# Kernel tuning notes

Measured on AMD Instinct MI355X. Metric: run time of the kernel, lower is better.

The kernel has to match this reference:

```python
import jax, jax.numpy as jnp
import numpy as np
import math

# config constants (match init_kwargs)
N_HEAD = 16
KNN_NUM = 4
MEM_FRAC = 4.0
BOOKKEEPING_FRAC = 0.0
RESID_ONLY = False
RESID_FOUND = 0.5   # set_resid_frac(resid_frac): found/current mix
RESID_CURR = 0.5
KNN_INFLUENCE = 1.0
NEG_INF = jnp.finfo(jnp.float32).min


def setup_inputs() -> dict:
    key = jax.random.key(0)
    k1, k2, k3, k4, k5 = jax.random.split(key, 5)
    B, T, C = 1, 2048, 1024
    H, d = N_HEAD, C // N_HEAD
    M = 8192  # per-head memory-store entries
    return {
        "x": jax.random.normal(k1, (B, T, C), jnp.float32),
        "c_attn_w": jax.random.normal(k2, (3 * C, C), jnp.float32) * 0.02,
        "c_proj_w": jax.random.normal(k3, (C, C), jnp.float32) * 0.02,
        "key_store": jax.random.normal(k4, (H, M, d), jnp.float32),
        "value_store": jax.random.normal(k5, (H, M, d), jnp.float32),
    }


def _knn_get(att, k, q, v, key_store, value_store):
    # att: (B,H,T,T), k/q/v: (B,H,T,d), stores: (H,M,d). B must be 1 (original
    # scatter offset i*t is only consistent for b==1).
    B, H, T, d = k.shape
    scale = 1.0 / math.sqrt(d)
    att_last = att[:, :, -1, :]                     # (B,H,T) last-query column
    # bookkeeping_frac == 0.0 -> skipped; mem_frac truthy -> threshold filter
    mask = att_last >= (1.0 / (MEM_FRAC * T))       # nonzero after zeroing

    # per-head flattened token lists, shape (H, N=B*T, d)
    kh = jnp.swapaxes(k, 0, 1).reshape(H, B * T, d)
    qh = jnp.swapaxes(q, 0, 1).reshape(H, B * T, d)
    vh = jnp.swapaxes(v, 0, 1).reshape(H, B * T, d)
    mask_h = jnp.swapaxes(mask, 0, 1).reshape(H, B * T)

    # exact L2 kNN (FAISS IndexFlatL2 equivalent): d2[h,n,m] = ||kh - ks||^2
    d2 = (jnp.sum(kh * kh, -1)[:, :, None]
          - 2.0 * jnp.einsum('hnd,hmd->hnm', kh, key_store)
          + jnp.sum(key_store * key_store, -1)[:, None, :])
    _, idx = jax.lax.top_k(-d2, KNN_NUM)            # (H,N,K) nearest indices

    h_ix = jnp.arange(H)[:, None, None]
    keys_found = key_store[h_ix, idx]               # (H,N,K,d)
    vals_found = value_store[h_ix, idx]
    keys_found = jnp.moveaxis(keys_found, 2, 0)     # (K,H,N,d)
    vals_found = jnp.moveaxis(vals_found, 2, 0)
    if not RESID_ONLY:
        keys_found = jnp.concatenate([kh[None], keys_found], axis=0)  # (K+1,H,N,d)
        vals_found = jnp.concatenate([vh[None], vals_found], axis=0)

    attf = jnp.einsum('khnd,hnd->khn', keys_found, qh) * scale
    attf = jnp.where(jnp.isnan(attf), NEG_INF, attf)
    attf = jax.nn.softmax(attf * KNN_INFLUENCE, axis=0)
    vals_new = jnp.einsum('khn,khnd->hnd', attf, vals_found)
    if RESID_FOUND > 0 or RESID_CURR > 0:
        vals_new = vals_new * RESID_FOUND + vh * RESID_CURR

    v_out = jnp.where(mask_h[..., None], vals_new, vh)   # scatter-equivalent
    return jnp.swapaxes(v_out.reshape(H, B, T, d), 0, 1)  # (B,H,T,d)


def reference(x, c_attn_w, c_proj_w, key_store, value_store):
    B, T, C = x.shape
    H, d = N_HEAD, C // N_HEAD
    qkv = x @ c_attn_w.T                             # (B,T,3C)
    q, k, v = jnp.split(qkv, 3, axis=2)
    q = jnp.swapaxes(q.reshape(B, T, H, d), 1, 2)    # (B,H,T,d)
    k = jnp.swapaxes(k.reshape(B, T, H, d), 1, 2)
    v = jnp.swapaxes(v.reshape(B, T, H, d), 1, 2)

    att = jnp.einsum('bhqd,bhkd->bhqk', q, k) * (1.0 / math.sqrt(d))
    causal = jnp.tril(jnp.ones((T, T), bool))
    att = jnp.where(causal, att, NEG_INF)
    att = jax.nn.softmax(att, axis=-1)

    # knn_get is @torch.no_grad() in the original -> stop_gradient
    v_new = jax.lax.stop_gradient(
        _knn_get(att, k, q, v, key_store, value_store))

    y = jnp.einsum('bhqk,bhkd->bhqd', att, v_new)
    y = jnp.swapaxes(y, 1, 2).reshape(B, T, C)
    return y @ c_proj_w.T
```

## Files before the change

### kernel.cpp

```cpp
#include <hip/hip_runtime.h>
#include <hip/hip_bf16.h>
#include <math.h>

#define TT 2048
#define CC 1024
#define HH 16
#define DDIM 64
#define MM 8192
#define C3 3072
#define SBIAS 256.0f

#define LTPAIR(sa,ma,sb,mb) ((sa) < (sb) || ((sa) == (sb) && (ma) < (mb)))

typedef __bf16 bf16x8 __attribute__((ext_vector_type(8)));
typedef float f32x4 __attribute__((ext_vector_type(4)));

__device__ __forceinline__ float waveReduceSum(float v) {
#pragma unroll
  for (int off = 32; off > 0; off >>= 1) v += __shfl_xor(v, off, 64);
  return v;
}
__device__ __forceinline__ unsigned waveMinU32(unsigned v) {
#pragma unroll
  for (int off = 32; off > 0; off >>= 1) {
    unsigned o = __shfl_xor(v, off, 64);
    v = (o < v) ? o : v;
  }
  return v;
}
__device__ __forceinline__ unsigned umn(unsigned a, unsigned b){ return a<b?a:b; }
__device__ __forceinline__ unsigned umx(unsigned a, unsigned b){ return a>b?a:b; }

__device__ __forceinline__ void gload16(const void* g, void* l) {
  __builtin_amdgcn_global_load_lds(
      (const __attribute__((address_space(1))) unsigned int*)g,
      (__attribute__((address_space(3))) unsigned int*)l, 16, 0, 0);
}

__global__ __launch_bounds__(256) void conv_split_k(const float* __restrict__ src,
    __hip_bfloat16* __restrict__ hi, __hip_bfloat16* __restrict__ lo)
{
  size_t i = (size_t)blockIdx.x*256 + threadIdx.x;
  const float4* p = (const float4*)(src + i*8);
  float4 a = p[0], b = p[1];
  float v[8] = {a.x,a.y,a.z,a.w,b.x,b.y,b.z,b.w};
  bf16x8 H, L;
#pragma unroll
  for (int e = 0; e < 8; ++e) {
    __bf16 hb = (__bf16)v[e];
    H[e] = hb;
    L[e] = (__bf16)(v[e] - (float)hb);
  }
  *reinterpret_cast<bf16x8*>(hi + i*8) = H;
  *reinterpret_cast<bf16x8*>(lo + i*8) = L;
}

__global__ __launch_bounds__(256) void conv_bf16_k(const float* __restrict__ src,
    __hip_bfloat16* __restrict__ dst)
{
  size_t i = (size_t)blockIdx.x*256 + threadIdx.x;
  const float4* p = (const float4*)(src + i*8);
  float4 a = p[0], b = p[1];
  float v[8] = {a.x,a.y,a.z,a.w,b.x,b.y,b.z,b.w};
  bf16x8 H;
#pragma unroll
  for (int e = 0; e < 8; ++e) H[e] = (__bf16)v[e];
  *reinterpret_cast<bf16x8*>(dst + i*8) = H;
}

__global__ __launch_bounds__(256) void conv_ks_k(const float* __restrict__ ks,
    __hip_bfloat16* __restrict__ ksb, float* __restrict__ ksn, float* __restrict__ ksnb)
{
  int row = blockIdx.x*4 + (threadIdx.x>>6);
  int lane = threadIdx.x & 63;
  float v = ks[(size_t)row*64 + lane];
  float sq = waveReduceSum(v*v);
  ksb[(size_t)row*64 + lane] = __float2bfloat16(v);
  if (lane == 0) { ksn[row] = sq; ksnb[row] = sq + SBIAS; }
}

__global__ __launch_bounds__(256) void conv_kb_k(const float* __restrict__ qkv,
    __hip_bfloat16* __restrict__ kb)
{
  int e = blockIdx.x*256 + threadIdx.x;
  int dg = e & 7; int t = (e>>3) & (TT-1); int h = e >> 14;
  const float* src = qkv + (size_t)t*C3 + CC + h*64 + dg*8;
  __hip_bfloat16* dst = kb + ((size_t)(h*TT + t)*64 + dg*8);
#pragma unroll
  for (int i = 0; i < 8; ++i) dst[i] = __float2bfloat16(src[i]);
}

__global__ __launch_bounds__(256) void vtrans_k(const float* __restrict__ vnew,
    __hip_bfloat16* __restrict__ vbT)
{
  __shared__ float tbuf[64][65];
  const int h = blockIdx.y, t0 = blockIdx.x*64, tid = threadIdx.x;
#pragma unroll
  for (int r = 0; r < 16; ++r) {
    int e = r*256 + tid; int row = e>>6, dv = e&63;
    tbuf[row][dv] = vnew[((size_t)h*TT + t0 + row)*64 + dv];
  }
  __syncthreads();
#pragma unroll
  for (int r = 0; r < 16; ++r) {
    int e = r*256 + tid; int dv = e>>6, tt = e&63;
    vbT[((size_t)h*64 + dv)*TT + t0 + tt] = __float2bfloat16(tbuf[tt][dv]);
  }
}

template<bool SPLIT>
__global__ __launch_bounds__(256) void gemm_mfma_k(
    const __hip_bfloat16* __restrict__ Ah, const __hip_bfloat16* __restrict__ Al,
    const __hip_bfloat16* __restrict__ Bh, const __hip_bfloat16* __restrict__ Bl,
    float* __restrict__ Cc, int M, int N, int K)
{
  __shared__ __align__(16) char lds[2][32768];
  const int tid = threadIdx.x;
  const int nbx = N >> 7;
  const int by = blockIdx.x / nbx, bx = blockIdx.x - by*nbx;
  const int m0 = by << 7, n0 = bx << 7;
  const int w = tid >> 6;
  const int l = tid & 63;
  const int wslot = w << 6;
  const int wi = w >> 1, wj = w & 1;
  const int fr = l & 15, fo = l >> 4;
  const int kw = SPLIT ? 32 : 64;
  const int nsteps = K / kw;

  f32x4 acc[4][4];
#pragma unroll
  for (int i = 0; i < 4; ++i)
#pragma unroll
    for (int j = 0; j < 4; ++j) acc[i][j] = f32x4{0.f,0.f,0.f,0.f};

  int srow[4], schg[4];
#pragma unroll
  for (int r = 0; r < 4; ++r) {
    int s = r*256 + tid;
    srow[r] = s >> 3;
    schg[r] = (s & 7) ^ (srow[r] & 7);
  }

  auto stageAB = [&](int buf, int st) {
    const int k0 = st * kw;
#pragma unroll
    for (int r = 0; r < 4; ++r) {
      const __hip_bfloat16 *pa, *pb;
      if (SPLIT) {
        pa = (schg[r] < 4 ? Ah : Al) + (size_t)(m0+srow[r])*K + k0 + (schg[r]&3)*8;
        pb = (schg[r] < 4 ? Bh : Bl) + (size_t)(n0+srow[r])*K + k0 + (schg[r]&3)*8;
      } else {
        pa = Ah + (size_t)(m0+srow[r])*K + k0 + schg[r]*8;
        pb = Bh + (size_t)(n0+srow[r])*K + k0 + schg[r]*8;
      }
      gload16(pa, lds[buf] + (r*256 + wslot)*16);
      gload16(pb, lds[buf] + 16384 + (r*256 + wslot)*16);
    }
  };

  stageAB(0, 0);
  __syncthreads();

  for (int st = 0; st < nsteps; ++st) {
    const int buf = st & 1;
    if (st + 1 < nsteps) stageAB(buf ^ 1, st + 1);
    char* ldsb = lds[buf];

    if (SPLIT) {
      bf16x8 bhf[4], blf[4];
#pragma unroll
      for (int j = 0; j < 4; ++j) {
        int row = wj*64 + j*16 + fr;
        bhf[j] = *(const bf16x8*)(ldsb + 16384 + row*128 + ((fo     ^ (row&7))*16));
        blf[j] = *(const bf16x8*)(ldsb + 16384 + row*128 + (((4+fo) ^ (row&7))*16));
      }
#pragma unroll
      for (int i = 0; i < 4; ++i) {
        int row = wi*64 + i*16 + fr;
        bf16x8 ah = *(const bf16x8*)(ldsb + row*128 + ((fo     ^ (row&7))*16));
        bf16x8 al = *(const bf16x8*)(ldsb + row*128 + (((4+fo) ^ (row&7))*16));
#pragma unroll
        for (int j = 0; j < 4; ++j) {
          acc[i][j] = __builtin_amdgcn_mfma_f32_16x16x32_bf16(al, bhf[j], acc[i][j], 0,0,0);
          acc[i][j] = __builtin_amdgcn_mfma_f32_16x16x32_bf16(ah, blf[j], acc[i][j], 0,0,0);
          acc[i][j] = __builtin_amdgcn_mfma_f32_16x16x32_bf16(ah, bhf[j], acc[i][j], 0,0,0);
        }
      }
    } else {
#pragma unroll
      for (int kk = 0; kk < 2; ++kk) {
        bf16x8 bf[4];
#pragma unroll
        for (int j = 0; j < 4; ++j) {
          int row = wj*64 + j*16 + fr;
          bf[j] = *(const bf16x8*)(ldsb + 16384 + row*128 + (((kk*4+fo) ^ (row&7))*16));
        }
#pragma unroll
        for (int i = 0; i < 4; ++i) {
          int row = wi*64 + i*16 + fr;
          bf16x8 af = *(const bf16x8*)(ldsb + row*128 + (((kk*4+fo) ^ (row&7))*16));
#pragma unroll
          for (int j = 0; j < 4; ++j)
            acc[i][j] = __builtin_amdgcn_mfma_f32_16x16x32_bf16(af, bf[j], acc[i][j], 0,0,0);
        }
      }
    }
    __syncthreads();
  }

  float* ep = (float*)((char*)lds + (size_t)w*8704);
#pragma unroll
  for (int pass = 0; pass < 2; ++pass) {
#pragma unroll
    for (int ii = 0; ii < 2; ++ii) {
      int i = pass*2 + ii;
#pragma unroll
      for (int j = 0; j < 4; ++j)
#pragma unroll
        for (int e = 0; e < 4; ++e)
          ep[(ii*16 + fo*4 + e)*68 + j*16 + fr] = acc[i][j][e];
    }
#pragma unroll
    for (int eidx = 0; eidx < 8; ++eidx) {
      int fi = eidx*64 + l;
      int row = fi >> 4, c4 = fi & 15;
      float4 v4 = *(const float4*)(ep + row*68 + c4*4);
      *(float4*)(Cc + (size_t)(m0 + wi*64 + pass*32 + row)*N + n0 + wj*64 + c4*4) = v4;
    }
  }
}

__global__ __launch_bounds__(256) void attlast_mask_k(const float* __restrict__ qkv, int* __restrict__ mask)
{
  const int h = blockIdx.x;
  __shared__ float ql[64];
  __shared__ float lg[TT];
  __shared__ float red[256];
  const int tid = threadIdx.x;
  if (tid < 64) ql[tid] = qkv[(size_t)(TT-1)*C3 + h*DDIM + tid];
  __syncthreads();
  float lmax = -INFINITY;
  for (int t = tid; t < TT; t += 256) {
    const float* kr = qkv + (size_t)t*C3 + CC + h*DDIM;
    float s = 0.f;
#pragma unroll
    for (int d = 0; d < 64; ++d) s += ql[d] * kr[d];
    s *= 0.125f;
    lg[t] = s;
    lmax = fmaxf(lmax, s);
  }
  red[tid] = lmax; __syncthreads();
  for (int off = 128; off > 0; off >>= 1) { if (tid < off) red[tid] = fmaxf(red[tid], red[tid+off]); __syncthreads(); }
  float mx = red[0];
  __syncthreads();
  float ls = 0.f;
  for (int t = tid; t < TT; t += 256) { float e = expf(lg[t]-mx); lg[t] = e; ls += e; }
  red[tid] = ls; __syncthreads();
  for (int off = 128; off > 0; off >>= 1) { if (tid < off) red[tid] += red[tid+off]; __syncthreads(); }
  float Z = red[0];
  for (int t = tid; t < TT; t += 256) mask[h*TT + t] = (lg[t]/Z >= 1.220703125e-4f) ? 1 : 0;
}

__global__ __launch_bounds__(256) void knn_chunkmin_k(
    const __hip_bfloat16* __restrict__ kb, const __hip_bfloat16* __restrict__ ksb,
    const float* __restrict__ ksnb, unsigned int* __restrict__ cand)
{
  __shared__ __align__(16) char lds[2*8192];
  const int tid = threadIdx.x;
  const int bid = blockIdx.x;
  const int orig = (bid & 7)*64 + (bid >> 3);
  const int h  = orig >> 5;
  const int n0 = (orig & 31) * 64;
  const int w  = tid >> 6;
  const int l  = tid & 63;
  const int cr = l & 15, hi = l >> 4;

  bf16x8 af0, af1;
  {
    const __hip_bfloat16* kbh = kb + (size_t)h*TT*64 + (size_t)(n0 + w*16 + cr)*64;
    af0 = *reinterpret_cast<const bf16x8*>(kbh + 0*32 + hi*8);
    af1 = *reinterpret_cast<const bf16x8*>(kbh + 1*32 + hi*8);
  }
  const __hip_bfloat16* ksbh = ksb + (size_t)h*MM*64;
  const float* ksnh = ksnb + (size_t)h*MM;

  const int c0 = tid*2, c1 = tid*2 + 1;
  const int wb0 = (c0>>3)*128 + (((c0&7) ^ ((c0>>3)&7))*16);
  const int wb1 = (c1>>3)*128 + (((c1&7) ^ ((c1>>3)&7))*16);
  const int rb0 = (l&15)*128 + (((0 + hi) ^ (l&7))*16);
  const int rb1 = (l&15)*128 + (((4 + hi) ^ (l&7))*16);

  unsigned cnd[4][4];
#pragma unroll
  for (int i = 0; i < 4; ++i)
#pragma unroll
    for (int c = 0; c < 4; ++c) cnd[i][c] = 0xFFFFFFFFu;

  uint4 r0, r1;
  {
    const uint4* g = reinterpret_cast<const uint4*>(ksbh);
    r0 = g[c0]; r1 = g[c1];
    *reinterpret_cast<uint4*>(lds + wb0) = r0;
    *reinterpret_cast<uint4*>(lds + wb1) = r1;
  }

  for (int tt = 0; tt < 128; ++tt) {
    __syncthreads();
    const int buf = tt & 1;
    char* ldsb = lds + buf*8192;
    if (tt + 1 < 128) {
      const uint4* g = reinterpret_cast<const uint4*>(ksbh + (size_t)(tt+1)*64*64);
      r0 = g[c0]; r1 = g[c1];
    }
    float kn0 = ksnh[tt*64 +  0 + cr];
    float kn1 = ksnh[tt*64 + 16 + cr];
    float kn2 = ksnh[tt*64 + 32 + cr];
    float kn3 = ksnh[tt*64 + 48 + cr];

    f32x4 acc[4];
#pragma unroll
    for (int b = 0; b < 4; ++b) {
      bf16x8 bf0 = *reinterpret_cast<const bf16x8*>(ldsb + b*2048 + rb0);
      bf16x8 bf1 = *reinterpret_cast<const bf16x8*>(ldsb + b*2048 + rb1);
      f32x4 z = {0.f, 0.f, 0.f, 0.f};
      z = __builtin_amdgcn_mfma_f32_16x16x32_bf16(af0, bf0, z, 0, 0, 0);
      z = __builtin_amdgcn_mfma_f32_16x16x32_bf16(af1, bf1, z, 0, 0, 0);
      acc[b] = z;
    }
#pragma unroll
    for (int i = 0; i < 4; ++i) {
      float s0 = fmaf(acc[0][i], -2.f, kn0);
      float s1 = fmaf(acc[1][i], -2.f, kn1);
      float s2 = fmaf(acc[2][i], -2.f, kn2);
      float s3 = fmaf(acc[3][i], -2.f, kn3);
      float m4 = fminf(fminf(s0, s1), fminf(s2, s3));
      unsigned x = (__float_as_uint(m4) & 0xFFFFFF80u) | (unsigned)tt;
      unsigned tmp;
      tmp = umn(cnd[i][0], x); x = umx(cnd[i][0], x); cnd[i][0] = tmp;
      tmp = umn(cnd[i][1], x); x = umx(cnd[i][1], x); cnd[i][1] = tmp;
      tmp = umn(cnd[i][2], x); x = umx(cnd[i][2], x); cnd[i][2] = tmp;
      cnd[i][3] = umn(cnd[i][3], x);
    }
    if (tt + 1 < 128) {
      char* ldsn = lds + (buf^1)*8192;
      *reinterpret_cast<uint4*>(ldsn + wb0) = r0;
      *reinterpret_cast<uint4*>(ldsn + wb1) = r1;
    }
  }

#pragma unroll
  for (int i = 0; i < 4; ++i) {
    int n = n0 + w*16 + hi*4 + i;
    reinterpret_cast<uint4*>(cand)[(size_t)(h*TT + n)*16 + cr] =
        make_uint4(cnd[i][0], cnd[i][1], cnd[i][2], cnd[i][3]);
  }
}

__global__ __launch_bounds__(256) void knn_select_k(
    const unsigned int* __restrict__ cand, const float* __restrict__ qkv,
    const float* __restrict__ kstore, const float* __restrict__ ksn,
    int* __restrict__ idxout)
{
  const int row = blockIdx.x*4 + (threadIdx.x>>6);
  const int l = threadIdx.x & 63;
  const int h = row >> 11, t = row & (TT-1);
  unsigned v = cand[(size_t)row*64 + (l&15)*4 + (l>>4)];
  const float kreg = qkv[(size_t)t*C3 + CC + h*64 + l];
  const float* ksh = kstore + (size_t)h*MM*64;
  const float* ksnh = ksn + (size_t)h*MM;

  float bs0=3.4e38f, bs1=3.4e38f, bs2=3.4e38f, bs3=3.4e38f;
  int bm0=0x7fffffff, bm1=0x7fffffff, bm2=0x7fffffff, bm3=0x7fffffff;

  for (int it = 0; it < 8; ++it) {
    unsigned mv = waveMinU32(v);
    if (mv == 0xFFFFFFFFu) break;
    unsigned long long ball = __ballot(v == mv);
    int src = __ffsll(ball) - 1;
    int tIdx = (int)(mv & 127u);
    int crw = src & 15;
    if (l == src) v = 0xFFFFFFFFu;
#pragma unroll
    for (int b = 0; b < 4; ++b) {
      int m = tIdx*64 + b*16 + crw;
      float ksv = ksh[(size_t)m*64 + l];
      float dot = waveReduceSum(kreg * ksv);
      float s = ksnh[m] - 2.f*dot;
      if (LTPAIR(s,m, bs3,bm3)) {
        if (LTPAIR(s,m, bs1,bm1)) {
          bs3=bs2; bm3=bm2; bs2=bs1; bm2=bm1;
          if (LTPAIR(s,m, bs0,bm0)) { bs1=bs0; bm1=bm0; bs0=s; bm0=m; }
          else { bs1=s; bm1=m; }
        } else {
          if (LTPAIR(s,m, bs2,bm2)) { bs3=bs2; bm3=bm2; bs2=s; bm2=m; }
          else { bs3=s; bm3=m; }
        }
      }
    }
  }
  if (l == 0) {
    int* o = idxout + (size_t)row*4;
    o[0]=bm0; o[1]=bm1; o[2]=bm2; o[3]=bm3;
  }
}

__global__ __launch_bounds__(256) void knn_apply_k(
    const float* __restrict__ qkv, const float* __restrict__ kstore, const float* __restrict__ vstore,
    const int* __restrict__ idx, const int* __restrict__ mask, float* __restrict__ vnew)
{
  const int r = blockIdx.x * 4 + (threadIdx.x >> 6);
  const int lane = threadIdx.x & 63;
  const int h = r >> 11, t = r & (TT-1);
  const float* base = qkv + (size_t)t*C3 + h*DDIM;
  float vh = base[2*CC + lane];
  float* outp = vnew + ((size_t)h*TT + t)*DDIM;
  if (!mask[r]) { outp[lane] = vh; return; }
  float qd = base[lane];
  float kd = base[CC + lane];
  float s0 = waveReduceSum(qd*kd) * 0.125f;
  float sj[4], vj[4];
#pragma unroll
  for (int j = 0; j < 4; ++j) {
    int m = idx[(size_t)r*4 + j];
    const float* kp = kstore + ((size_t)h*MM + m)*DDIM;
    const float* vp = vstore + ((size_t)h*MM + m)*DDIM;
    sj[j] = waveReduceSum(qd * kp[lane]) * 0.125f;
    vj[j] = vp[lane];
  }
  float mx = fmaxf(fmaxf(fmaxf(s0,sj[0]),fmaxf(sj[1],sj[2])),sj[3]);
  float w0 = expf(s0-mx), w1 = expf(sj[0]-mx), w2 = expf(sj[1]-mx), w3 = expf(sj[2]-mx), w4 = expf(sj[3]-mx);
  float Z = w0+w1+w2+w3+w4;
  float vnw = (w0*vh + w1*vj[0] + w2*vj[1] + w3*vj[2] + w4*vj[3]) / Z;
  outp[lane] = 0.5f*vnw + 0.5f*vh;
}

__global__ __launch_bounds__(256) void attn_mfma_k(
    const float* __restrict__ qkv, const __hip_bfloat16* __restrict__ kb,
    const __hip_bfloat16* __restrict__ vbT, __hip_bfloat16* __restrict__ yb)
{
  __shared__ __align__(16) char lds[40960];
  const int h = blockIdx.y, bx = blockIdx.x, tid = threadIdx.x;
  const int w = tid>>6, l = tid&63, fr = l&15, fo = l>>4;
  const int wslot = w << 6;
  const __hip_bfloat16* kbh = kb + (size_t)h*TT*64;
  const __hip_bfloat16* vbh = vbT + (size_t)h*64*TT;
  char* Pt = lds + 32768 + w*2048;

  int srow[2], schg[2];
#pragma unroll
  for (int r = 0; r < 2; ++r) {
    int s = r*256 + tid;
    srow[r] = s >> 3;
    schg[r] = (s & 7) ^ (srow[r] & 7);
  }

  auto stageKV = [&](int buf, int kt) {
#pragma unroll
    for (int r = 0; r < 2; ++r) {
      gload16(kbh + (size_t)(kt*64 + srow[r])*64 + schg[r]*8,
              lds + buf*16384 + (r*256 + wslot)*16);
      gload16(vbh + (size_t)srow[r]*TT + kt*64 + schg[r]*8,
              lds + buf*16384 + 8192 + (r*256 + wslot)*16);
    }
  };

  for (int half = 0; half < 2; ++half) {
    const int qblk = half ? (31 - bx) : bx;
    const int q0 = qblk * 64;
    bf16x8 qa[2];
    {
      const float* qrow = qkv + (size_t)(q0 + w*16 + fr)*C3 + h*64;
#pragma unroll
      for (int kk = 0; kk < 2; ++kk) {
        float4 u0 = *(const float4*)(qrow + kk*32 + fo*8);
        float4 u1 = *(const float4*)(qrow + kk*32 + fo*8 + 4);
        bf16x8 t;
        t[0]=(__bf16)u0.x; t[1]=(__bf16)u0.y; t[2]=(__bf16)u0.z; t[3]=(__bf16)u0.w;
        t[4]=(__bf16)u1.x; t[5]=(__bf16)u1.y; t[6]=(__bf16)u1.z; t[7]=(__bf16)u1.w;
        qa[kk] = t;
      }
    }
    float mrow[4], lsum[4];
    f32x4 oacc[4];
#pragma unroll
    for (int e = 0; e < 4; ++e) { mrow[e] = -INFINITY; lsum[e] = 0.f; }
#pragma unroll
    for (int jv = 0; jv < 4; ++jv) oacc[jv] = f32x4{0.f,0.f,0.f,0.f};

    const int ntiles = qblk + 1;
    stageKV(0, 0);
    __syncthreads();

    for (int kt = 0; kt < ntiles; ++kt) {
      const int buf = kt & 1;
      if (kt + 1 < ntiles) stageKV(buf ^ 1, kt + 1);
      char* Kt = lds + buf*16384;
      char* Vt = Kt + 8192;

      f32x4 sv[4];
#pragma unroll
      for (int j = 0; j < 4; ++j) {
        int row = j*16 + fr;
        bf16x8 k0f = *(const bf16x8*)(Kt + row*128 + ((fo     ^ (row&7))*16));
        bf16x8 k1f = *(const bf16x8*)(Kt + row*128 + (((4+fo) ^ (row&7))*16));
        f32x4 z = {0.f,0.f,0.f,0.f};
        z = __builtin_amdgcn_mfma_f32_16x16x32_bf16(qa[0], k0f, z, 0,0,0);
        z = __builtin_amdgcn_mfma_f32_16x16x32_bf16(qa[1], k1f, z, 0,0,0);
        sv[j] = z;
      }
      if (kt == qblk) {
#pragma unroll
        for (int j = 0; j < 4; ++j)
#pragma unroll
          for (int e = 0; e < 4; ++e)
            sv[j][e] = (j*16 + fr <= w*16 + fo*4 + e) ? sv[j][e]*0.125f : -INFINITY;
      } else {
#pragma unroll
        for (int j = 0; j < 4; ++j)
#pragma unroll
          for (int e = 0; e < 4; ++e) sv[j][e] *= 0.125f;
      }
      float rmax[4];
#pragma unroll
      for (int e = 0; e < 4; ++e)
        rmax[e] = fmaxf(fmaxf(sv[0][e], sv[1][e]), fmaxf(sv[2][e], sv[3][e]));
#pragma unroll
      for (int off = 1; off < 16; off <<= 1)
#pragma unroll
        for (int e = 0; e < 4; ++e) rmax[e] = fmaxf(rmax[e], __shfl_xor(rmax[e], off, 64));
      float scl[4];
#pragma unroll
      for (int e = 0; e < 4; ++e) {
        float mn = fmaxf(mrow[e], rmax[e]);
        scl[e] = __expf(mrow[e] - mn);
        mrow[e] = mn;
      }
      float rsum[4] = {0.f,0.f,0.f,0.f};
#pragma unroll
      for (int j = 0; j < 4; ++j) {
        int chunkbase = j*2 + (fr>>3);
        int kvoff = (fr&7)*2;
#pragma unroll
        for (int e = 0; e < 4; ++e) {
          float p = __expf(sv[j][e] - mrow[e]);
          rsum[e] += p;
          int qloc = fo*4 + e;
          *(__bf16*)(Pt + qloc*128 + ((chunkbase ^ (qloc&7))*16) + kvoff) = (__bf16)p;
        }
      }
#pragma unroll
      for (int off = 1; off < 16; off <<= 1)
#pragma unroll
        for (int e = 0; e < 4; ++e) rsum[e] += __shfl_xor(rsum[e], off, 64);
#pragma unroll
      for (int e = 0; e < 4; ++e) lsum[e] = lsum[e]*scl[e] + rsum[e];
#pragma unroll
      for (int jv = 0; jv < 4; ++jv)
#pragma unroll
        for (int e = 0; e < 4; ++e) oacc[jv][e] *= scl[e];

      bf16x8 pa0 = *(const bf16x8*)(Pt + fr*128 + ((fo     ^ (fr&7))*16));
      bf16x8 pa1 = *(const bf16x8*)(Pt + fr*128 + (((4+fo) ^ (fr&7))*16));
#pragma unroll
      for (int jv = 0; jv < 4; ++jv) {
        int row = jv*16 + fr;
        bf16x8 v0f = *(const bf16x8*)(Vt + row*128 + ((fo     ^ (row&7))*16));
        bf16x8 v1f = *(const bf16x8*)(Vt + row*128 + (((4+fo) ^ (row&7))*16));
        oacc[jv] = __builtin_amdgcn_mfma_f32_16x16x32_bf16(pa0, v0f, oacc[jv], 0,0,0);
        oacc[jv] = __builtin_amdgcn_mfma_f32_16x16x32_bf16(pa1, v1f, oacc[jv], 0,0,0);
      }
      __syncthreads();
    }
#pragma unroll
    for (int jv = 0; jv < 4; ++jv)
#pragma unroll
      for (int e = 0; e < 4; ++e) {
        int t = q0 + w*16 + fo*4 + e;
        yb[(size_t)t*CC + h*64 + jv*16 + fr] = __float2bfloat16(oacc[jv][e] / lsum[e]);
      }
  }
}

extern "C" void kernel_launch(void* const* d_in, const int* in_sizes, int n_in,
                              void* d_out, int out_size, void* d_ws, size_t ws_size,
                              hipStream_t stream) {
  const float* x   = (const float*)d_in[0];
  const float* wat = (const float*)d_in[1];
  const float* wpr = (const float*)d_in[2];
  const float* kst = (const float*)d_in[3];
  const float* vst = (const float*)d_in[4];
  float* out = (float*)d_out;

  float* ws    = (float*)d_ws;
  float* qkv   = ws;
  float* ksn   = qkv + (size_t)6291456;
  float* ksnb  = ksn + 131072;
  int*   idxb  = (int*)(ksnb + 131072);
  int*   maskb = idxb + 131072;
  __hip_bfloat16* kb = (__hip_bfloat16*)(maskb + 32768);
  float* candRegion = (float*)kb + 1048576;
  unsigned int* candb = (unsigned int*)candRegion;
  float* vnew = candRegion;
  __hip_bfloat16* vbT = (__hip_bfloat16*)(candRegion + 2097152);
  float* split = candRegion + 2097152 + 1048576;
  __hip_bfloat16* xhi = (__hip_bfloat16*)split;
  __hip_bfloat16* xlo = xhi + 2097152;
  __hip_bfloat16* whi = xlo + 2097152;
  __hip_bfloat16* wlo = whi + 3145728;
  __hip_bfloat16* ksb  = (__hip_bfloat16*)split;
  __hip_bfloat16* wprb = ksb + 8388608;
  __hip_bfloat16* yb   = (__hip_bfloat16*)split;

  conv_split_k<<<dim3(1024), 256, 0, stream>>>(x, xhi, xlo);
  conv_split_k<<<dim3(1536), 256, 0, stream>>>(wat, whi, wlo);
  gemm_mfma_k<true><<<dim3(16*24), 256, 0, stream>>>(xhi, xlo, whi, wlo, qkv, TT, C3, CC);
  conv_kb_k<<<dim3(1024), 256, 0, stream>>>(qkv, kb);
  conv_ks_k<<<dim3(HH*MM/4), 256, 0, stream>>>(kst, ksb, ksn, ksnb);
  conv_bf16_k<<<dim3(512), 256, 0, stream>>>(wpr, wprb);
  attlast_mask_k<<<dim3(HH), 256, 0, stream>>>(qkv, maskb);
  knn_chunkmin_k<<<dim3(512), 256, 0, stream>>>(kb, ksb, ksnb, candb);
  knn_select_k<<<dim3(HH*TT/4), 256, 0, stream>>>(candb, qkv, kst, ksn, idxb);
  knn_apply_k<<<dim3(HH*TT/4), 256, 0, stream>>>(qkv, kst, vst, idxb, maskb, vnew);
  vtrans_k<<<dim3(32, HH), 256, 0, stream>>>(vnew, vbT);
  attn_mfma_k<<<dim3(16, HH), 256, 0, stream>>>(qkv, kb, vbT, yb);
  gemm_mfma_k<false><<<dim3(16*8), 256, 0, stream>>>(yb, nullptr, wprb, nullptr, out, TT, CC, CC);
}
```

Measured before the change: 352.4 us.

## Fuse kNN select and apply kernels with wave-wide bitonic candidate sort

Merges the kNN candidate-selection and value-apply kernels into one kernel and skips the selection work for rows whose mask is zero. The serial 8-iteration wave-min loop, with its per-candidate wave reductions, is replaced by a bitonic sort across the wave. Each lane pair then computes one exact fp32 distance, and a second bitonic sort on (score, index) keys picks the top four. The candidate encoding now packs the column-within-chunk bits into the key, which lowers the float precision kept in the first-pass ranking. That could change which candidates reach exact rescoring. It also drops the intermediate index buffer and one kernel launch.

```diff
diff --git a/kernel.cpp b/kernel.cpp
--- a/kernel.cpp
+++ b/kernel.cpp
@@ -10,22 +10,12 @@
 #define C3 3072
 #define SBIAS 256.0f
 
-#define LTPAIR(sa,ma,sb,mb) ((sa) < (sb) || ((sa) == (sb) && (ma) < (mb)))
-
 typedef __bf16 bf16x8 __attribute__((ext_vector_type(8)));
 typedef float f32x4 __attribute__((ext_vector_type(4)));
 
 __device__ __forceinline__ float waveReduceSum(float v) {
 #pragma unroll
   for (int off = 32; off > 0; off >>= 1) v += __shfl_xor(v, off, 64);
-  return v;
-}
-__device__ __forceinline__ unsigned waveMinU32(unsigned v) {
-#pragma unroll
-  for (int off = 32; off > 0; off >>= 1) {
-    unsigned o = __shfl_xor(v, off, 64);
-    v = (o < v) ? o : v;
-  }
   return v;
 }
 __device__ __forceinline__ unsigned umn(unsigned a, unsigned b){ return a<b?a:b; }
@@ -274,6 +264,7 @@
   const int w  = tid >> 6;
   const int l  = tid & 63;
   const int cr = l & 15, hi = l >> 4;
+  const unsigned crbits = (unsigned)cr << 7;
 
   bf16x8 af0, af1;
   {
@@ -334,7 +325,7 @@
       float s2 = fmaf(acc[2][i], -2.f, kn2);
       float s3 = fmaf(acc[3][i], -2.f, kn3);
       float m4 = fminf(fminf(s0, s1), fminf(s2, s3));
-      unsigned x = (__float_as_uint(m4) & 0xFFFFFF80u) | (unsigned)tt;
+      unsigned x = (__float_as_uint(m4) & 0xFFFFF800u) | crbits | (unsigned)tt;
       unsigned tmp;
       tmp = umn(cnd[i][0], x); x = umx(cnd[i][0], x); cnd[i][0] = tmp;
       tmp = umn(cnd[i][1], x); x = umx(cnd[i][1], x); cnd[i][1] = tmp;
@@ -356,82 +347,100 @@
   }
 }
 
-__global__ __launch_bounds__(256) void knn_select_k(
+__global__ __launch_bounds__(256) void knn_fused_k(
     const unsigned int* __restrict__ cand, const float* __restrict__ qkv,
-    const float* __restrict__ kstore, const float* __restrict__ ksn,
-    int* __restrict__ idxout)
+    const float* __restrict__ kstore, const float* __restrict__ vstore,
+    const float* __restrict__ ksn, const int* __restrict__ mask,
+    float* __restrict__ vnew)
 {
   const int row = blockIdx.x*4 + (threadIdx.x>>6);
   const int l = threadIdx.x & 63;
   const int h = row >> 11, t = row & (TT-1);
-  unsigned v = cand[(size_t)row*64 + (l&15)*4 + (l>>4)];
-  const float kreg = qkv[(size_t)t*C3 + CC + h*64 + l];
-  const float* ksh = kstore + (size_t)h*MM*64;
-  const float* ksnh = ksn + (size_t)h*MM;
-
-  float bs0=3.4e38f, bs1=3.4e38f, bs2=3.4e38f, bs3=3.4e38f;
-  int bm0=0x7fffffff, bm1=0x7fffffff, bm2=0x7fffffff, bm3=0x7fffffff;
-
-  for (int it = 0; it < 8; ++it) {
-    unsigned mv = waveMinU32(v);
-    if (mv == 0xFFFFFFFFu) break;
-    unsigned long long ball = __ballot(v == mv);
-    int src = __ffsll(ball) - 1;
-    int tIdx = (int)(mv & 127u);
-    int crw = src & 15;
-    if (l == src) v = 0xFFFFFFFFu;
-#pragma unroll
-    for (int b = 0; b < 4; ++b) {
-      int m = tIdx*64 + b*16 + crw;
-      float ksv = ksh[(size_t)m*64 + l];
-      float dot = waveReduceSum(kreg * ksv);
-      float s = ksnh[m] - 2.f*dot;
-      if (LTPAIR(s,m, bs3,bm3)) {
-        if (LTPAIR(s,m, bs1,bm1)) {
-          bs3=bs2; bm3=bm2; bs2=bs1; bm2=bm1;
-          if (LTPAIR(s,m, bs0,bm0)) { bs1=bs0; bm1=bm0; bs0=s; bm0=m; }
-          else { bs1=s; bm1=m; }
-        } else {
-          if (LTPAIR(s,m, bs2,bm2)) { bs3=bs2; bm3=bm2; bs2=s; bm2=m; }
-          else { bs3=s; bm3=m; }
-        }
-      }
-    }
-  }
-  if (l == 0) {
-    int* o = idxout + (size_t)row*4;
-    o[0]=bm0; o[1]=bm1; o[2]=bm2; o[3]=bm3;
-  }
-}
-
-__global__ __launch_bounds__(256) void knn_apply_k(
-    const float* __restrict__ qkv, const float* __restrict__ kstore, const float* __restrict__ vstore,
-    const int* __restrict__ idx, const int* __restrict__ mask, float* __restrict__ vnew)
-{
-  const int r = blockIdx.x * 4 + (threadIdx.x >> 6);
-  const int lane = threadIdx.x & 63;
-  const int h = r >> 11, t = r & (TT-1);
-  const float* base = qkv + (size_t)t*C3 + h*DDIM;
-  float vh = base[2*CC + lane];
-  float* outp = vnew + ((size_t)h*TT + t)*DDIM;
-  if (!mask[r]) { outp[lane] = vh; return; }
-  float qd = base[lane];
-  float kd = base[CC + lane];
-  float s0 = waveReduceSum(qd*kd) * 0.125f;
-  float sj[4], vj[4];
-#pragma unroll
-  for (int j = 0; j < 4; ++j) {
-    int m = idx[(size_t)r*4 + j];
-    const float* kp = kstore + ((size_t)h*MM + m)*DDIM;
-    const float* vp = vstore + ((size_t)h*MM + m)*DDIM;
-    sj[j] = waveReduceSum(qd * kp[lane]) * 0.125f;
-    vj[j] = vp[lane];
-  }
-  float mx = fmaxf(fmaxf(fmaxf(s0,sj[0]),fmaxf(sj[1],sj[2])),sj[3]);
-  float w0 = expf(s0-mx), w1 = expf(sj[0]-mx), w2 = expf(sj[1]-mx), w3 = expf(sj[2]-mx), w4 = expf(sj[3]-mx);
+  const float* base = qkv + (size_t)t*C3 + h*64;
+  float vh = base[2*CC + l];
+  float* outp = vnew + (size_t)row*64;
+  if (!mask[row]) { outp[l] = vh; return; }
+
+  unsigned v = cand[(size_t)row*64 + l];
+#pragma unroll
+  for (int k = 2; k <= 64; k <<= 1)
+#pragma unroll
+    for (int j = k>>1; j > 0; j >>= 1) {
+      unsigned o = __shfl_xor(v, j, 64);
+      bool takeMin = ((l & j) == 0) == ((l & k) == 0);
+      v = (takeMin == (o < v)) ? o : v;
+    }
+
+  const int c = l >> 1;
+  const int b = c & 3;
+  unsigned vc = __shfl(v, c >> 2, 64);
+  const int m = ((int)(vc & 127u))*64 + b*16 + (int)((vc >> 7) & 15u);
+  const int p = l & 1;
+  {
+    const float* kq = base + CC + p*32;
+    const float* ksr = kstore + ((size_t)h*MM + m)*64 + p*32;
+    float dp = 0.f;
+#pragma unroll
+    for (int i = 0; i < 8; ++i) {
+      float4 a = *(const float4*)(kq + i*4);
+      float4 bb = *(const float4*)(ksr + i*4);
+      dp = fmaf(a.x,bb.x, fmaf(a.y,bb.y, fmaf(a.z,bb.z, fmaf(a.w,bb.w, dp))));
+    }
+    dp += __shfl_xor(dp, 1, 64);
+    float s = ksn[(size_t)h*MM + m] - 2.f*dp;
+    unsigned u = __float_as_uint(s);
+    unsigned skey = u ^ (unsigned)(((int)u >> 31) | 0x80000000);
+    unsigned khi = (p == 0) ? skey : 0xFFFFFFFFu;
+    unsigned klo = (p == 0) ? (unsigned)m : 0xFFFFFFFFu;
+#pragma unroll
+    for (int k = 2; k <= 64; k <<= 1)
+#pragma unroll
+      for (int j = k>>1; j > 0; j >>= 1) {
+        unsigned oh = __shfl_xor(khi, j, 64);
+        unsigned ol = __shfl_xor(klo, j, 64);
+        bool takeMin = ((l & j) == 0) == ((l & k) == 0);
+        bool oLess = (oh < khi) || (oh == khi && ol < klo);
+        if (takeMin == oLess) { khi = oh; klo = ol; }
+      }
+    v = klo;
+  }
+
+  const int m0 = (int)__shfl(v, 0, 64);
+  const int m1 = (int)__shfl(v, 1, 64);
+  const int m2 = (int)__shfl(v, 2, 64);
+  const int m3 = (int)__shfl(v, 3, 64);
+  const int g = l >> 3, gl = l & 7;
+  float dq = 0.f;
+  if (g < 5) {
+    int msel = (g == 0) ? m0 : (g == 1) ? m1 : (g == 2) ? m2 : m3;
+    const float* qrow = base + gl*8;
+    const float* kr = (g < 4) ? (kstore + ((size_t)h*MM + msel)*64 + gl*8)
+                              : (base + CC + gl*8);
+    float4 a0 = *(const float4*)(qrow);
+    float4 a1 = *(const float4*)(qrow + 4);
+    float4 b0 = *(const float4*)(kr);
+    float4 b1 = *(const float4*)(kr + 4);
+    dq = a0.x*b0.x + a0.y*b0.y + a0.z*b0.z + a0.w*b0.w
+       + a1.x*b1.x + a1.y*b1.y + a1.z*b1.z + a1.w*b1.w;
+  }
+  dq += __shfl_xor(dq, 1, 64);
+  dq += __shfl_xor(dq, 2, 64);
+  dq += __shfl_xor(dq, 4, 64);
+  float d0 = __shfl(dq,  0, 64)*0.125f;
+  float d1 = __shfl(dq,  8, 64)*0.125f;
+  float d2 = __shfl(dq, 16, 64)*0.125f;
+  float d3 = __shfl(dq, 24, 64)*0.125f;
+  float d4 = __shfl(dq, 32, 64)*0.125f;
+  float mx = fmaxf(fmaxf(fmaxf(d0,d1),fmaxf(d2,d3)),d4);
+  float w0 = expf(d0-mx), w1 = expf(d1-mx), w2 = expf(d2-mx),
+        w3 = expf(d3-mx), w4 = expf(d4-mx);
   float Z = w0+w1+w2+w3+w4;
-  float vnw = (w0*vh + w1*vj[0] + w2*vj[1] + w3*vj[2] + w4*vj[3]) / Z;
-  outp[lane] = 0.5f*vnw + 0.5f*vh;
+  float vv = w4*vh
+           + w0*vstore[((size_t)h*MM+m0)*64 + l]
+           + w1*vstore[((size_t)h*MM+m1)*64 + l]
+           + w2*vstore[((size_t)h*MM+m2)*64 + l]
+           + w3*vstore[((size_t)h*MM+m3)*64 + l];
+  outp[l] = 0.5f*(vv/Z) + 0.5f*vh;
 }
 
 __global__ __launch_bounds__(256) void attn_mfma_k(
@@ -619,8 +628,7 @@
   conv_bf16_k<<<dim3(512), 256, 0, stream>>>(wpr, wprb);
   attlast_mask_k<<<dim3(HH), 256, 0, stream>>>(qkv, maskb);
   knn_chunkmin_k<<<dim3(512), 256, 0, stream>>>(kb, ksb, ksnb, candb);
-  knn_select_k<<<dim3(HH*TT/4), 256, 0, stream>>>(candb, qkv, kst, ksn, idxb);
-  knn_apply_k<<<dim3(HH*TT/4), 256, 0, stream>>>(qkv, kst, vst, idxb, maskb, vnew);
+  knn_fused_k<<<dim3(HH*TT/4), 256, 0, stream>>>(candb, qkv, kst, vst, ksn, maskb, vnew);
   vtrans_k<<<dim3(32, HH), 256, 0, stream>>>(vnew, vbT);
   attn_mfma_k<<<dim3(16, HH), 256, 0, stream>>>(qkv, kb, vbT, yb);
   gemm_mfma_k<false><<<dim3(16*8), 256, 0, stream>>>(yb, nullptr, wprb, nullptr, out, TT, CC, CC);
```

Measured after the change: 314.2 us. 1.12x faster.
